# Performance work log

Hardware: AMD Instinct MI355X
Metric: run time of the kernel (lower is better)

Reference implementation:

```python
import jax, jax.numpy as jnp
import numpy as np

DIM = 512
HEADS = 8
HEAD_DIM = 64
MAX_FREQ = 256.0


def axial_freqs(H, W, head_dim, max_freq=MAX_FREQ):
    # rotary-embedding-torch: per-axis rotary dim = head_dim // 2, freqs_for='pixel'
    r = head_dim // 2
    base = jnp.linspace(1.0, max_freq / 2.0, r // 2) * jnp.pi  # (r/2,)
    ph = jnp.linspace(-1.0, 1.0, H)
    pw = jnp.linspace(-1.0, 1.0, W)
    fh = jnp.repeat(ph[:, None] * base[None, :], 2, axis=-1)  # (H, r) interleaved repeat
    fw = jnp.repeat(pw[:, None] * base[None, :], 2, axis=-1)  # (W, r)
    fh = jnp.broadcast_to(fh[:, None, :], (H, W, r))
    fw = jnp.broadcast_to(fw[None, :, :], (H, W, r))
    return jnp.concatenate([fh, fw], axis=-1)  # (H, W, head_dim)


def rotate_half(t):
    # interleaved pairs: (x1, x2) -> (-x2, x1)
    shp = t.shape
    t = t.reshape(*shp[:-1], -1, 2)
    return jnp.stack((-t[..., 1], t[..., 0]), axis=-1).reshape(shp)


def apply_rope(t, freqs):
    # freqs: (H, W, d) broadcast over (BT, h, H, W, d)
    return t * jnp.cos(freqs) + rotate_half(t) * jnp.sin(freqs)


def setup_inputs() -> dict:
    key = jax.random.key(0)
    k1, k2, k3 = jax.random.split(key, 3)
    B, T, H, W, D = 2, 8, 32, 32, DIM
    inner = HEADS * HEAD_DIM
    x = jax.random.normal(k1, (B, T, H, W, D), dtype=jnp.float32)
    w_qkv = jax.random.normal(k2, (3 * inner, D), dtype=jnp.float32) * (D ** -0.5)
    w_out = jax.random.normal(k3, (D, inner), dtype=jnp.float32) * (inner ** -0.5)
    b_out = jnp.zeros((D,), dtype=jnp.float32)
    return {"x": x, "w_qkv": w_qkv, "w_out": w_out, "b_out": b_out}


def reference(x, w_qkv, w_out, b_out):
    B, T, H, W, D = x.shape
    h, d = HEADS, HEAD_DIM
    qkv = jnp.einsum('bthwc,fc->bthwf', x, w_qkv)  # (B,T,H,W,3*inner)
    q, k, v = jnp.split(qkv, 3, axis=-1)

    def to_heads(t):
        # B T H W (h d) -> (B T) h H W d
        t = t.reshape(B * T, H, W, h, d)
        return jnp.transpose(t, (0, 3, 1, 2, 4))

    q, k, v = to_heads(q), to_heads(k), to_heads(v)
    freqs = axial_freqs(H, W, d)
    q = apply_rope(q, freqs)
    k = apply_rope(k, freqs)

    q = q.reshape(B * T, h, H * W, d)
    k = k.reshape(B * T, h, H * W, d)
    v = v.reshape(B * T, h, H * W, d)

    scale = d ** -0.5
    logits = jnp.einsum('bhnd,bhmd->bhnm', q, k) * scale
    attn = jax.nn.softmax(logits, axis=-1)
    out = jnp.einsum('bhnm,bhmd->bhnd', attn, v)  # (BT, h, HW, d)

    # (B T) h (H W) d -> B T H W (h d)
    out = out.reshape(B, T, h, H, W, d)
    out = jnp.transpose(out, (0, 1, 3, 4, 2, 5)).reshape(B, T, H, W, h * d)
    return jnp.einsum('bthwf,df->bthwd', out, w_out) + b_out
```

## Files before the change

### kernel.cpp

```cpp
#include <hip/hip_runtime.h>
#include <math.h>

#define NH 8
#define HD 64
#define NSEQ 1024
#define DMODEL 512
#define F3 1536
#define NTOK 16384
#define BH 128
#define KVP 72
#define TP 136
#define QSCALE 0.1803368867f

typedef __attribute__((ext_vector_type(8))) short bf16x8;
typedef __attribute__((ext_vector_type(4))) float f32x4;
typedef __attribute__((ext_vector_type(16))) float f32x16;
typedef __attribute__((ext_vector_type(4))) unsigned int u32x4;
#define MFMA16(a, b, c) __builtin_amdgcn_mfma_f32_16x16x32_bf16(a, b, c, 0, 0, 0)
#define MFMA32(a, b, c) __builtin_amdgcn_mfma_f32_32x32x16_bf16(a, b, c, 0, 0, 0)

__device__ __forceinline__ float freq_of(int j) {
    return 3.14159265358979323846f * (1.0f + (float)j * (127.0f / 15.0f));
}
__device__ __forceinline__ unsigned short bf16_hi(float x) {
    unsigned u = __builtin_bit_cast(unsigned, x);
    return (unsigned short)(u >> 16);
}
__device__ __forceinline__ unsigned short bf16_rtn(float x) {
    unsigned u = __builtin_bit_cast(unsigned, x);
    return (unsigned short)((u + 0x7FFF + ((u >> 16) & 1)) >> 16);
}
__device__ __forceinline__ float bf16_tofloat(unsigned short h) {
    unsigned u = ((unsigned)h) << 16;
    return __builtin_bit_cast(float, u);
}
__device__ __forceinline__ int swz(int r) { return (r & 3) ^ ((r >> 2) & 3); }

__global__ __launch_bounds__(256) void cvt_kernel(
        const float* __restrict__ src, unsigned short* __restrict__ dst) {
    const int i = blockIdx.x * 256 + threadIdx.x;
    const float4 v = ((const float4*)src)[i];
    ((ushort4*)dst)[i] = make_ushort4(bf16_rtn(v.x), bf16_rtn(v.y),
                                      bf16_rtn(v.z), bf16_rtn(v.w));
}

template<int PLANES, int NREP>
__device__ __forceinline__ void gemm_reg_pipe(
        const unsigned short* __restrict__ a_hi, const unsigned short* __restrict__ a_lo,
        const unsigned short* __restrict__ b_bf,
        char* lds, int m0, int f0, int t, f32x4 (&acc)[NREP][4][4]) {
    const int w = t >> 6, lane = t & 63, l15 = lane & 15, quad = lane >> 4;
    const int mw = (w & 1) * 64, nw = (w >> 1) * 64;
    const int APL = PLANES - 1;
    const int NPL = APL + NREP;
    const int STAGE = NPL * 4096;
    const int r = t >> 1;
    const int g0 = (t & 1) * 2;

    uint4 regs[NPL][2];
    auto load_regs = [&](int kt) {
        const int k0 = kt * 32;
        #pragma unroll
        for (int p = 0; p < NPL; p++) {
            const unsigned short* src = (p < APL) ? (p == 0 ? a_hi : a_lo) : b_bf;
            const int row0 = (p < APL) ? m0 : (f0 + (p - APL) * 128);
            const unsigned short* g = src + (size_t)(row0 + r) * DMODEL + k0 + g0 * 8;
            regs[p][0] = *(const uint4*)g;
            regs[p][1] = *(const uint4*)(g + 8);
        }
    };
    auto store_lds = [&](int stage) {
        unsigned short* S = (unsigned short*)lds + stage * STAGE;
        const int s0 = ((g0 ^ swz(r))) * 8;
        const int s1 = (((g0 + 1) ^ swz(r))) * 8;
        #pragma unroll
        for (int p = 0; p < NPL; p++) {
            unsigned short* Sp = S + p * 4096 + r * 32;
            *(uint4*)&Sp[s0] = regs[p][0];
            *(uint4*)&Sp[s1] = regs[p][1];
        }
    };

    load_regs(0);
    store_lds(0);
    for (int kt = 0; kt < 16; kt++) {
        __syncthreads();
        if (kt < 15) load_regs(kt + 1);
        const unsigned short* S = (const unsigned short*)lds + (kt & 1) * STAGE;
        bf16x8 ah[4], al[4];
        #pragma unroll
        for (int mt = 0; mt < 4; mt++) {
            const int rr = mw + mt * 16 + l15;
            const int off = rr * 32 + (quad ^ swz(rr)) * 8;
            ah[mt] = *(const bf16x8*)&S[off];
            if (APL == 2) al[mt] = *(const bf16x8*)&S[4096 + off];
        }
        #pragma unroll
        for (int nr = 0; nr < NREP; nr++) {
            bf16x8 bb[4];
            #pragma unroll
            for (int nt = 0; nt < 4; nt++) {
                const int rr = nw + nt * 16 + l15;
                bb[nt] = *(const bf16x8*)&S[(APL + nr) * 4096 + rr * 32
                                            + (quad ^ swz(rr)) * 8];
            }
            #pragma unroll
            for (int mt = 0; mt < 4; mt++)
                #pragma unroll
                for (int nt = 0; nt < 4; nt++) {
                    acc[nr][mt][nt] = MFMA16(ah[mt], bb[nt], acc[nr][mt][nt]);
                    if (APL == 2) acc[nr][mt][nt] = MFMA16(al[mt], bb[nt], acc[nr][mt][nt]);
                }
        }
        if (kt < 15) store_lds((kt + 1) & 1);
    }
    __syncthreads();
}

__device__ __forceinline__ void gemm_pipe_qkv(
        const float* __restrict__ x, const unsigned short* __restrict__ b_bf,
        char* lds, int m0, int f0, int t, f32x4 (&acc)[2][4][4]) {
    const int w = t >> 6, lane = t & 63, l15 = lane & 15, quad = lane >> 4;
    const int mw = (w & 1) * 64, nw = (w >> 1) * 64;
    const int STAGE = 4 * 4096;
    const int r = t >> 1;
    const int g0 = (t & 1) * 2;

    float4 af[4];
    uint4 bregs[2][2];
    auto load_regs = [&](int kt) {
        const int k0 = kt * 32;
        const float* gA = x + (size_t)(m0 + r) * DMODEL + k0 + g0 * 8;
        #pragma unroll
        for (int i = 0; i < 4; i++) af[i] = ((const float4*)gA)[i];
        #pragma unroll
        for (int p = 0; p < 2; p++) {
            const unsigned short* g =
                b_bf + (size_t)(f0 + p * 128 + r) * DMODEL + k0 + g0 * 8;
            bregs[p][0] = *(const uint4*)g;
            bregs[p][1] = *(const uint4*)(g + 8);
        }
    };
    auto store_lds = [&](int stage) {
        unsigned short* S = (unsigned short*)lds + stage * STAGE;
        const int s0 = ((g0 ^ swz(r))) * 8;
        const int s1 = (((g0 + 1) ^ swz(r))) * 8;
        auto cvt8 = [](const float4 a, const float4 b, uint4& hq, uint4& lq) {
            const float f[8] = {a.x, a.y, a.z, a.w, b.x, b.y, b.z, b.w};
            unsigned hw[4], lw[4];
            #pragma unroll
            for (int j = 0; j < 4; j++) {
                const unsigned u0 = __builtin_bit_cast(unsigned, f[2 * j]);
                const unsigned u1 = __builtin_bit_cast(unsigned, f[2 * j + 1]);
                const float r0 = f[2 * j]     - __builtin_bit_cast(float, u0 & 0xFFFF0000u);
                const float r1 = f[2 * j + 1] - __builtin_bit_cast(float, u1 & 0xFFFF0000u);
                hw[j] = (u0 >> 16) | (u1 & 0xFFFF0000u);
                lw[j] = (__builtin_bit_cast(unsigned, r0) >> 16)
                      | (__builtin_bit_cast(unsigned, r1) & 0xFFFF0000u);
            }
            hq = make_uint4(hw[0], hw[1], hw[2], hw[3]);
            lq = make_uint4(lw[0], lw[1], lw[2], lw[3]);
        };
        uint4 h0, l0, h1, l1;
        cvt8(af[0], af[1], h0, l0);
        cvt8(af[2], af[3], h1, l1);
        unsigned short* Sh = S + r * 32;
        unsigned short* Sl = S + 4096 + r * 32;
        *(uint4*)&Sh[s0] = h0; *(uint4*)&Sh[s1] = h1;
        *(uint4*)&Sl[s0] = l0; *(uint4*)&Sl[s1] = l1;
        #pragma unroll
        for (int p = 0; p < 2; p++) {
            unsigned short* Sp = S + (2 + p) * 4096 + r * 32;
            *(uint4*)&Sp[s0] = bregs[p][0];
            *(uint4*)&Sp[s1] = bregs[p][1];
        }
    };

    load_regs(0);
    store_lds(0);
    for (int kt = 0; kt < 16; kt++) {
        __syncthreads();
        if (kt < 15) load_regs(kt + 1);
        const unsigned short* S = (const unsigned short*)lds + (kt & 1) * STAGE;
        bf16x8 ah[4], al[4];
        #pragma unroll
        for (int mt = 0; mt < 4; mt++) {
            const int rr = mw + mt * 16 + l15;
            const int off = rr * 32 + (quad ^ swz(rr)) * 8;
            ah[mt] = *(const bf16x8*)&S[off];
            al[mt] = *(const bf16x8*)&S[4096 + off];
        }
        #pragma unroll
        for (int nr = 0; nr < 2; nr++) {
            bf16x8 bb[4];
            #pragma unroll
            for (int nt = 0; nt < 4; nt++) {
                const int rr = nw + nt * 16 + l15;
                bb[nt] = *(const bf16x8*)&S[(2 + nr) * 4096 + rr * 32
                                            + (quad ^ swz(rr)) * 8];
            }
            #pragma unroll
            for (int mt = 0; mt < 4; mt++)
                #pragma unroll
                for (int nt = 0; nt < 4; nt++) {
                    acc[nr][mt][nt] = MFMA16(ah[mt], bb[nt], acc[nr][mt][nt]);
                    acc[nr][mt][nt] = MFMA16(al[mt], bb[nt], acc[nr][mt][nt]);
                }
        }
        if (kt < 15) store_lds((kt + 1) & 1);
    }
    __syncthreads();
}

__global__ __launch_bounds__(256, 2) void qkv_mfma_kernel(
        const float* __restrict__ x, const unsigned short* __restrict__ wq_bf,
        unsigned short* __restrict__ q_bf, unsigned short* __restrict__ k_bf,
        unsigned short* __restrict__ v_th) {
    __shared__ __align__(16) char lds[65536 + 4608];
    unsigned short* T = (unsigned short*)lds;
    float* t_cy = (float*)(lds + 65536);
    float* t_sy = t_cy + 64;
    float* t_cx = t_sy + 64;
    float* t_sx = t_cx + 512;

    const int m0 = blockIdx.x * 128;
    const int f0 = blockIdx.y * 256;
    const int t = threadIdx.x;
    const int w = t >> 6, lane = t & 63, l15 = lane & 15, quad = lane >> 4;
    const int mw = (w & 1) * 64, nw = (w >> 1) * 64;
    const int sel = f0 >> 9;
    const int bt = m0 >> 10;
    const int n0 = m0 & 1023;

    if (sel != 2) {
        for (int idx = t; idx < 576; idx += 256) {
            if (idx < 64) {
                const int yi = idx >> 4, j = idx & 15;
                const float pos = -1.0f + (float)((n0 >> 5) + yi) * (2.0f / 31.0f);
                float sv, cv; sincosf(pos * freq_of(j), &sv, &cv);
                t_sy[idx] = sv; t_cy[idx] = cv;
            } else {
                const int k2 = idx - 64, xi = k2 >> 4, j = k2 & 15;
                const float pos = -1.0f + (float)xi * (2.0f / 31.0f);
                float sv, cv; sincosf(pos * freq_of(j), &sv, &cv);
                t_sx[k2] = sv; t_cx[k2] = cv;
            }
        }
    }
    __syncthreads();

    f32x4 acc[2][4][4];
    #pragma unroll
    for (int nr = 0; nr < 2; nr++)
        #pragma unroll
        for (int mt = 0; mt < 4; mt++)
            #pragma unroll
            for (int nt = 0; nt < 4; nt++) acc[nr][mt][nt] = (f32x4){0.f, 0.f, 0.f, 0.f};

    gemm_pipe_qkv(x, wq_bf, lds, m0, f0, t, acc);

    #pragma unroll
    for (int nr = 0; nr < 2; nr++) {
        const int fs = f0 + nr * 128;
        if (sel != 2) {
            const float post = (sel == 0) ? QSCALE : 1.0f;
            #pragma unroll
            for (int mt = 0; mt < 4; mt++)
                #pragma unroll
                for (int nt = 0; nt < 4; nt++)
                    #pragma unroll
                    for (int rr = 0; rr < 4; rr++) {
                        const int ml = mw + mt * 16 + quad * 4 + rr;
                        const int dd = (nw + nt * 16 + l15) & 63;
                        const int j0 = (dd & 31) >> 1;
                        float c, s;
                        if (dd < 32) { c = t_cy[(ml >> 5) * 16 + j0]; s = t_sy[(ml >> 5) * 16 + j0]; }
                        else         { c = t_cx[(ml & 31) * 16 + j0]; s = t_sx[(ml & 31) * 16 + j0]; }
                        const float v = acc[nr][mt][nt][rr];
                        const float pv = __shfl_xor(v, 1);
                        acc[nr][mt][nt][rr] =
                            ((l15 & 1) ? (v * c + pv * s) : (v * c - pv * s)) * post;
                    }
        }

        if (sel == 2) {
            #pragma unroll
            for (int mt = 0; mt < 4; mt++)
                #pragma unroll
                for (int nt = 0; nt < 4; nt++) {
                    const int fl = nw + nt * 16 + l15;
                    const int mlb = mw + mt * 16 + quad * 4;
                    ushort4 pk = make_ushort4(
                        bf16_rtn(acc[nr][mt][nt][0]), bf16_rtn(acc[nr][mt][nt][1]),
                        bf16_rtn(acc[nr][mt][nt][2]), bf16_rtn(acc[nr][mt][nt][3]));
                    *(ushort4*)&T[fl * TP + mlb] = pk;
                }
        } else {
            #pragma unroll
            for (int mt = 0; mt < 4; mt++)
                #pragma unroll
                for (int nt = 0; nt < 4; nt++)
                    #pragma unroll
                    for (int rr = 0; rr < 4; rr++) {
                        const int ml = mw + mt * 16 + quad * 4 + rr;
                        const int fl = nw + nt * 16 + l15;
                        T[ml * TP + fl] = bf16_rtn(acc[nr][mt][nt][rr]);
                    }
        }
        __syncthreads();
        if (sel == 2) {
            #pragma unroll
            for (int p = 0; p < 8; p++) {
                const int idx = p * 256 + t;
                const int fl = idx >> 4, g8 = (idx & 15) * 8;
                const int head = ((fs + fl) >> 6) & 7;
                *(uint4*)(v_th + ((size_t)(bt * NH + head) * HD + ((fs + fl) & 63)) * NSEQ
                          + n0 + g8) = *(const uint4*)&T[fl * TP + g8];
            }
        } else {
            unsigned short* dst = (sel == 0) ? q_bf : k_bf;
            #pragma unroll
            for (int p = 0; p < 8; p++) {
                const int idx = p * 256 + t;
                const int ml = idx >> 4, g8 = (idx & 15) * 8;
                const int head = ((fs + g8) >> 6) & 7;
                *(uint4*)(dst + ((size_t)(bt * NH + head) * NSEQ + n0 + ml) * HD
                          + ((fs + g8) & 63)) = *(const uint4*)&T[ml * TP + g8];
            }
        }
        __syncthreads();
    }
}

__global__ __launch_bounds__(256, 3) void attn_kernel(
        const unsigned short* __restrict__ q_bf, const unsigned short* __restrict__ k_bf,
        const unsigned short* __restrict__ v_th,
        unsigned short* __restrict__ o_bf) {
    __shared__ unsigned short Ks[2][64 * KVP];
    __shared__ unsigned short Vs[2][64 * KVP];

    const int bh = blockIdx.x;
    const int qt = blockIdx.y;
    const int t = threadIdx.x;
    const int w = t >> 6;
    const int lane = t & 63;
    const int l31 = lane & 31;
    const int hi = lane >> 5;

    const size_t bh_nd = (size_t)bh * NSEQ * HD;
    const size_t bh_dn = (size_t)bh * HD * NSEQ;

    bf16x8 qfB[4];
    {
        const size_t rbase = bh_nd + (size_t)(qt * 128 + w * 32 + l31) * HD + hi * 8;
        #pragma unroll
        for (int ds = 0; ds < 4; ds++)
            qfB[ds] = *(const bf16x8*)(q_bf + rbase + ds * 16);
    }

    uint4 kr[2], vr[2];
    auto load_kv = [&](int kt) {
        #pragma unroll
        for (int p = 0; p < 2; p++) {
            const int cc = t + p * 256;
            const int r = cc >> 3, off8 = (cc & 7) * 8;
            kr[p] = *(const uint4*)(k_bf + bh_nd + (size_t)(kt * 64 + r) * HD + off8);
            vr[p] = *(const uint4*)(v_th + bh_dn + (size_t)r * NSEQ + kt * 64 + off8);
        }
    };
    auto store_kv = [&](int st) {
        #pragma unroll
        for (int p = 0; p < 2; p++) {
            const int cc = t + p * 256;
            const int r = cc >> 3, off8 = (cc & 7) * 8;
            *(uint4*)&Ks[st][r * KVP + off8] = kr[p];
            *(uint4*)&Vs[st][r * KVP + off8] = vr[p];
        }
    };

    const bf16x8 ones = {(short)0x3F80, (short)0x3F80, (short)0x3F80, (short)0x3F80,
                         (short)0x3F80, (short)0x3F80, (short)0x3F80, (short)0x3F80};

    f32x16 o_acc[2], l_acc;
    #pragma unroll
    for (int i = 0; i < 16; i++) {
        o_acc[0][i] = 0.f; o_acc[1][i] = 0.f; l_acc[i] = 0.f;
    }

    load_kv(0);
    store_kv(0);
    for (int kt = 0; kt < 16; kt++) {
        __syncthreads();
        if (kt < 15) load_kv(kt + 1);
        const unsigned short* K = Ks[kt & 1];
        const unsigned short* V = Vs[kt & 1];

        #pragma unroll
        for (int nt2 = 0; nt2 < 2; nt2++) {
            f32x16 s;
            #pragma unroll
            for (int i = 0; i < 16; i++) s[i] = 0.f;
            #pragma unroll
            for (int ds = 0; ds < 4; ds++) {
                const bf16x8 kb =
                    *(const bf16x8*)&K[(nt2 * 32 + l31) * KVP + ds * 16 + hi * 8];
                s = MFMA32(kb, qfB[ds], s);
            }

            unsigned wv[8];
            #pragma unroll
            for (int i = 0; i < 8; i++) {
                const float p0 = exp2f(s[2 * i]);
                const float p1 = exp2f(s[2 * i + 1]);
                asm("v_cvt_pk_bf16_f32 %0, %1, %2" : "=v"(wv[i]) : "v"(p0), "v"(p1));
            }
            asm volatile("v_permlane32_swap_b32 %0, %1" : "+v"(wv[0]), "+v"(wv[2]));
            asm volatile("v_permlane32_swap_b32 %0, %1" : "+v"(wv[1]), "+v"(wv[3]));
            asm volatile("v_permlane32_swap_b32 %0, %1" : "+v"(wv[4]), "+v"(wv[6]));
            asm volatile("v_permlane32_swap_b32 %0, %1" : "+v"(wv[5]), "+v"(wv[7]));

            #pragma unroll
            for (int k2 = 0; k2 < 2; k2++) {
                const u32x4 paw = {wv[k2 * 4 + 0], wv[k2 * 4 + 1],
                                   wv[k2 * 4 + 2], wv[k2 * 4 + 3]};
                const bf16x8 pa = __builtin_bit_cast(bf16x8, paw);
                const int kstep = nt2 * 2 + k2;
                l_acc = MFMA32(pa, ones, l_acc);
                #pragma unroll
                for (int dt = 0; dt < 2; dt++) {
                    const bf16x8 vb =
                        *(const bf16x8*)&V[(dt * 32 + l31) * KVP + kstep * 16 + hi * 8];
                    o_acc[dt] = MFMA32(pa, vb, o_acc[dt]);
                }
            }
        }
        if (kt < 15) store_kv((kt + 1) & 1);
    }

    __syncthreads();
    unsigned short* Osh = &Ks[0][0];
    #pragma unroll
    for (int r = 0; r < 16; r++) {
        const float inv = 1.0f / l_acc[r];
        const int row = w * 32 + (r & 3) + 8 * (r >> 2) + 4 * hi;
        #pragma unroll
        for (int dt = 0; dt < 2; dt++)
            Osh[row * KVP + dt * 32 + l31] = bf16_rtn(o_acc[dt][r] * inv);
    }
    __syncthreads();
    const int btq = bh >> 3, head = bh & 7;
    #pragma unroll
    for (int p = 0; p < 4; p++) {
        const int idx = p * 256 + t;
        const int row = idx >> 3, g8 = (idx & 7) * 8;
        *(uint4*)(o_bf + ((size_t)(btq * NSEQ + qt * 128 + row)) * DMODEL
                  + head * HD + g8) = *(const uint4*)&Osh[row * KVP + g8];
    }
}

__global__ __launch_bounds__(256, 3) void proj_mfma_kernel(
        const unsigned short* __restrict__ o_bf,
        const unsigned short* __restrict__ wo_bf,
        const float* __restrict__ b_out, float* __restrict__ out) {
    __shared__ __align__(16) char lds[32768];

    const int m0 = blockIdx.x * 128;
    const int f0 = blockIdx.y * 128;
    const int t = threadIdx.x;
    const int w = t >> 6, lane = t & 63, l15 = lane & 15, quad = lane >> 4;
    const int mw = (w & 1) * 64, nw = (w >> 1) * 64;

    f32x4 acc[1][4][4];
    #pragma unroll
    for (int mt = 0; mt < 4; mt++)
        #pragma unroll
        for (int nt = 0; nt < 4; nt++) acc[0][mt][nt] = (f32x4){0.f, 0.f, 0.f, 0.f};

    gemm_reg_pipe<2, 1>(o_bf, o_bf, wo_bf, lds, m0, f0, t, acc);

    float bias_v[4];
    #pragma unroll
    for (int nt = 0; nt < 4; nt++) bias_v[nt] = b_out[f0 + nw + nt * 16 + l15];
    #pragma unroll
    for (int mt = 0; mt < 4; mt++)
        #pragma unroll
        for (int nt = 0; nt < 4; nt++)
            #pragma unroll
            for (int rr = 0; rr < 4; rr++) {
                const int m = m0 + mw + mt * 16 + quad * 4 + rr;
                out[(size_t)m * DMODEL + f0 + nw + nt * 16 + l15] =
                    acc[0][mt][nt][rr] + bias_v[nt];
            }
}

extern "C" void kernel_launch(void* const* d_in, const int* in_sizes, int n_in,
                              void* d_out, int out_size, void* d_ws, size_t ws_size,
                              hipStream_t stream) {
    const float* x  = (const float*)d_in[0];
    const float* wq = (const float*)d_in[1];
    const float* wo = (const float*)d_in[2];
    const float* bo = (const float*)d_in[3];
    float* out = (float*)d_out;

    const size_t per = (size_t)BH * NSEQ * HD;
    unsigned short* o_bf = (unsigned short*)d_ws;
    unsigned short* q_bf = o_bf + per;
    unsigned short* k_bf = q_bf + per;
    unsigned short* v_th = k_bf + per;
    unsigned short* wq_bf = v_th + per;
    unsigned short* wo_bf = wq_bf + (size_t)F3 * DMODEL;

    cvt_kernel<<<dim3(F3 * DMODEL / 1024), 256, 0, stream>>>(wq, wq_bf);
    cvt_kernel<<<dim3(DMODEL * DMODEL / 1024), 256, 0, stream>>>(wo, wo_bf);
    qkv_mfma_kernel<<<dim3(NTOK / 128, F3 / 256), 256, 0, stream>>>(
        x, wq_bf, q_bf, k_bf, v_th);
    attn_kernel<<<dim3(BH, 8), 256, 0, stream>>>(
        q_bf, k_bf, v_th, o_bf);
    proj_mfma_kernel<<<dim3(NTOK / 128, DMODEL / 128), 256, 0, stream>>>(
        o_bf, wo_bf, bo, out);
}
```

Before: 250.5 us.

## Double per-block query tile in attention, widen proj N tile, merge weight converts

Each attention wave now processes two 32-row query fragments, so every K and V fragment loaded from LDS feeds twice as many MFMAs, and the grid halves to 4 query tiles of 256 rows. The output projection now computes a 128x256 tile per block using the register pipeline with two N replicas, and its LDS grows to 48KB. The two weight-conversion launches are merged into a single kernel. The cost is more registers (launch bounds lowered to 2 blocks per SM), lower occupancy, and fewer blocks for the GPU to schedule.

Measured after the change: 234.3 us. -6.5%, faster.

```diff
diff --git a/kernel.cpp b/kernel.cpp
--- a/kernel.cpp
+++ b/kernel.cpp
@@ -22,23 +22,21 @@
 __device__ __forceinline__ float freq_of(int j) {
     return 3.14159265358979323846f * (1.0f + (float)j * (127.0f / 15.0f));
 }
-__device__ __forceinline__ unsigned short bf16_hi(float x) {
-    unsigned u = __builtin_bit_cast(unsigned, x);
-    return (unsigned short)(u >> 16);
-}
 __device__ __forceinline__ unsigned short bf16_rtn(float x) {
     unsigned u = __builtin_bit_cast(unsigned, x);
     return (unsigned short)((u + 0x7FFF + ((u >> 16) & 1)) >> 16);
 }
-__device__ __forceinline__ float bf16_tofloat(unsigned short h) {
-    unsigned u = ((unsigned)h) << 16;
-    return __builtin_bit_cast(float, u);
-}
 __device__ __forceinline__ int swz(int r) { return (r & 3) ^ ((r >> 2) & 3); }
 
-__global__ __launch_bounds__(256) void cvt_kernel(
-        const float* __restrict__ src, unsigned short* __restrict__ dst) {
-    const int i = blockIdx.x * 256 + threadIdx.x;
+__global__ __launch_bounds__(256) void cvt2_kernel(
+        const float* __restrict__ wq, unsigned short* __restrict__ wq_bf,
+        const float* __restrict__ wo, unsigned short* __restrict__ wo_bf) {
+    const int b = blockIdx.x;
+    const float* src;
+    unsigned short* dst;
+    int i;
+    if (b < F3 * DMODEL / 1024) { src = wq; dst = wq_bf; i = b * 256 + threadIdx.x; }
+    else { src = wo; dst = wo_bf; i = (b - F3 * DMODEL / 1024) * 256 + threadIdx.x; }
     const float4 v = ((const float4*)src)[i];
     ((ushort4*)dst)[i] = make_ushort4(bf16_rtn(v.x), bf16_rtn(v.y),
                                       bf16_rtn(v.z), bf16_rtn(v.w));
@@ -332,7 +330,7 @@
     }
 }
 
-__global__ __launch_bounds__(256, 3) void attn_kernel(
+__global__ __launch_bounds__(256, 2) void attn_kernel(
         const unsigned short* __restrict__ q_bf, const unsigned short* __restrict__ k_bf,
         const unsigned short* __restrict__ v_th,
         unsigned short* __restrict__ o_bf) {
@@ -350,12 +348,14 @@
     const size_t bh_nd = (size_t)bh * NSEQ * HD;
     const size_t bh_dn = (size_t)bh * HD * NSEQ;
 
-    bf16x8 qfB[4];
-    {
-        const size_t rbase = bh_nd + (size_t)(qt * 128 + w * 32 + l31) * HD + hi * 8;
+    bf16x8 qfB[2][4];
+    #pragma unroll
+    for (int mf = 0; mf < 2; mf++) {
+        const size_t rbase =
+            bh_nd + (size_t)(qt * 256 + w * 64 + mf * 32 + l31) * HD + hi * 8;
         #pragma unroll
         for (int ds = 0; ds < 4; ds++)
-            qfB[ds] = *(const bf16x8*)(q_bf + rbase + ds * 16);
+            qfB[mf][ds] = *(const bf16x8*)(q_bf + rbase + ds * 16);
     }
 
     uint4 kr[2], vr[2];
@@ -381,10 +381,12 @@
     const bf16x8 ones = {(short)0x3F80, (short)0x3F80, (short)0x3F80, (short)0x3F80,
                          (short)0x3F80, (short)0x3F80, (short)0x3F80, (short)0x3F80};
 
-    f32x16 o_acc[2], l_acc;
+    f32x16 o_acc[2][2], l_acc[2];
     #pragma unroll
     for (int i = 0; i < 16; i++) {
-        o_acc[0][i] = 0.f; o_acc[1][i] = 0.f; l_acc[i] = 0.f;
+        o_acc[0][0][i] = 0.f; o_acc[0][1][i] = 0.f;
+        o_acc[1][0][i] = 0.f; o_acc[1][1][i] = 0.f;
+        l_acc[0][i] = 0.f; l_acc[1][i] = 0.f;
     }
 
     load_kv(0);
@@ -397,40 +399,49 @@
 
         #pragma unroll
         for (int nt2 = 0; nt2 < 2; nt2++) {
-            f32x16 s;
-            #pragma unroll
-            for (int i = 0; i < 16; i++) s[i] = 0.f;
-            #pragma unroll
-            for (int ds = 0; ds < 4; ds++) {
-                const bf16x8 kb =
-                    *(const bf16x8*)&K[(nt2 * 32 + l31) * KVP + ds * 16 + hi * 8];
-                s = MFMA32(kb, qfB[ds], s);
-            }
-
-            unsigned wv[8];
-            #pragma unroll
-            for (int i = 0; i < 8; i++) {
-                const float p0 = exp2f(s[2 * i]);
-                const float p1 = exp2f(s[2 * i + 1]);
-                asm("v_cvt_pk_bf16_f32 %0, %1, %2" : "=v"(wv[i]) : "v"(p0), "v"(p1));
-            }
-            asm volatile("v_permlane32_swap_b32 %0, %1" : "+v"(wv[0]), "+v"(wv[2]));
-            asm volatile("v_permlane32_swap_b32 %0, %1" : "+v"(wv[1]), "+v"(wv[3]));
-            asm volatile("v_permlane32_swap_b32 %0, %1" : "+v"(wv[4]), "+v"(wv[6]));
-            asm volatile("v_permlane32_swap_b32 %0, %1" : "+v"(wv[5]), "+v"(wv[7]));
+            bf16x8 kb[4];
+            #pragma unroll
+            for (int ds = 0; ds < 4; ds++)
+                kb[ds] = *(const bf16x8*)&K[(nt2 * 32 + l31) * KVP + ds * 16 + hi * 8];
+
+            u32x4 paw[2][2];
+            #pragma unroll
+            for (int mf = 0; mf < 2; mf++) {
+                f32x16 s;
+                #pragma unroll
+                for (int i = 0; i < 16; i++) s[i] = 0.f;
+                #pragma unroll
+                for (int ds = 0; ds < 4; ds++) s = MFMA32(kb[ds], qfB[mf][ds], s);
+
+                unsigned wv[8];
+                #pragma unroll
+                for (int i = 0; i < 8; i++) {
+                    const float p0 = exp2f(s[2 * i]);
+                    const float p1 = exp2f(s[2 * i + 1]);
+                    asm("v_cvt_pk_bf16_f32 %0, %1, %2" : "=v"(wv[i]) : "v"(p0), "v"(p1));
+                }
+                asm volatile("v_permlane32_swap_b32 %0, %1" : "+v"(wv[0]), "+v"(wv[2]));
+                asm volatile("v_permlane32_swap_b32 %0, %1" : "+v"(wv[1]), "+v"(wv[3]));
+                asm volatile("v_permlane32_swap_b32 %0, %1" : "+v"(wv[4]), "+v"(wv[6]));
+                asm volatile("v_permlane32_swap_b32 %0, %1" : "+v"(wv[5]), "+v"(wv[7]));
+                paw[mf][0] = (u32x4){wv[0], wv[1], wv[2], wv[3]};
+                paw[mf][1] = (u32x4){wv[4], wv[5], wv[6], wv[7]};
+            }
 
             #pragma unroll
             for (int k2 = 0; k2 < 2; k2++) {
-                const u32x4 paw = {wv[k2 * 4 + 0], wv[k2 * 4 + 1],
-                                   wv[k2 * 4 + 2], wv[k2 * 4 + 3]};
-                const bf16x8 pa = __builtin_bit_cast(bf16x8, paw);
-                const int kstep = nt2 * 2 + k2;
-                l_acc = MFMA32(pa, ones, l_acc);
-                #pragma unroll
-                for (int dt = 0; dt < 2; dt++) {
-                    const bf16x8 vb =
-                        *(const bf16x8*)&V[(dt * 32 + l31) * KVP + kstep * 16 + hi * 8];
-                    o_acc[dt] = MFMA32(pa, vb, o_acc[dt]);
+                bf16x8 vb[2];
+                #pragma unroll
+                for (int dt = 0; dt < 2; dt++)
+                    vb[dt] = *(const bf16x8*)&V[(dt * 32 + l31) * KVP
+                                 + (nt2 * 2 + k2) * 16 + hi * 8];
+                #pragma unroll
+                for (int mf = 0; mf < 2; mf++) {
+                    const bf16x8 pa = __builtin_bit_cast(bf16x8, paw[mf][k2]);
+                    l_acc[mf] = MFMA32(pa, ones, l_acc[mf]);
+                    #pragma unroll
+                    for (int dt = 0; dt < 2; dt++)
+                        o_acc[mf][dt] = MFMA32(pa, vb[dt], o_acc[mf][dt]);
                 }
             }
         }
@@ -440,57 +451,65 @@
     __syncthreads();
     unsigned short* Osh = &Ks[0][0];
     #pragma unroll
-    for (int r = 0; r < 16; r++) {
-        const float inv = 1.0f / l_acc[r];
-        const int row = w * 32 + (r & 3) + 8 * (r >> 2) + 4 * hi;
-        #pragma unroll
-        for (int dt = 0; dt < 2; dt++)
-            Osh[row * KVP + dt * 32 + l31] = bf16_rtn(o_acc[dt][r] * inv);
-    }
+    for (int mf = 0; mf < 2; mf++)
+        #pragma unroll
+        for (int r = 0; r < 16; r++) {
+            const float inv = 1.0f / l_acc[mf][r];
+            const int row = w * 64 + mf * 32 + (r & 3) + 8 * (r >> 2) + 4 * hi;
+            #pragma unroll
+            for (int dt = 0; dt < 2; dt++)
+                Osh[row * KVP + dt * 32 + l31] = bf16_rtn(o_acc[mf][dt][r] * inv);
+        }
     __syncthreads();
     const int btq = bh >> 3, head = bh & 7;
     #pragma unroll
-    for (int p = 0; p < 4; p++) {
+    for (int p = 0; p < 8; p++) {
         const int idx = p * 256 + t;
         const int row = idx >> 3, g8 = (idx & 7) * 8;
-        *(uint4*)(o_bf + ((size_t)(btq * NSEQ + qt * 128 + row)) * DMODEL
+        *(uint4*)(o_bf + ((size_t)(btq * NSEQ + qt * 256 + row)) * DMODEL
                   + head * HD + g8) = *(const uint4*)&Osh[row * KVP + g8];
     }
 }
 
-__global__ __launch_bounds__(256, 3) void proj_mfma_kernel(
+__global__ __launch_bounds__(256, 2) void proj_mfma_kernel(
         const unsigned short* __restrict__ o_bf,
         const unsigned short* __restrict__ wo_bf,
         const float* __restrict__ b_out, float* __restrict__ out) {
-    __shared__ __align__(16) char lds[32768];
+    __shared__ __align__(16) char lds[49152];
 
     const int m0 = blockIdx.x * 128;
-    const int f0 = blockIdx.y * 128;
+    const int f0 = blockIdx.y * 256;
     const int t = threadIdx.x;
     const int w = t >> 6, lane = t & 63, l15 = lane & 15, quad = lane >> 4;
     const int mw = (w & 1) * 64, nw = (w >> 1) * 64;
 
-    f32x4 acc[1][4][4];
-    #pragma unroll
-    for (int mt = 0; mt < 4; mt++)
-        #pragma unroll
-        for (int nt = 0; nt < 4; nt++) acc[0][mt][nt] = (f32x4){0.f, 0.f, 0.f, 0.f};
-
-    gemm_reg_pipe<2, 1>(o_bf, o_bf, wo_bf, lds, m0, f0, t, acc);
-
-    float bias_v[4];
-    #pragma unroll
-    for (int nt = 0; nt < 4; nt++) bias_v[nt] = b_out[f0 + nw + nt * 16 + l15];
-    #pragma unroll
-    for (int mt = 0; mt < 4; mt++)
-        #pragma unroll
-        for (int nt = 0; nt < 4; nt++)
-            #pragma unroll
-            for (int rr = 0; rr < 4; rr++) {
-                const int m = m0 + mw + mt * 16 + quad * 4 + rr;
-                out[(size_t)m * DMODEL + f0 + nw + nt * 16 + l15] =
-                    acc[0][mt][nt][rr] + bias_v[nt];
-            }
+    f32x4 acc[2][4][4];
+    #pragma unroll
+    for (int nr = 0; nr < 2; nr++)
+        #pragma unroll
+        for (int mt = 0; mt < 4; mt++)
+            #pragma unroll
+            for (int nt = 0; nt < 4; nt++) acc[nr][mt][nt] = (f32x4){0.f, 0.f, 0.f, 0.f};
+
+    gemm_reg_pipe<2, 2>(o_bf, o_bf, wo_bf, lds, m0, f0, t, acc);
+
+    #pragma unroll
+    for (int nr = 0; nr < 2; nr++) {
+        const int fs = f0 + nr * 128;
+        float bias_v[4];
+        #pragma unroll
+        for (int nt = 0; nt < 4; nt++) bias_v[nt] = b_out[fs + nw + nt * 16 + l15];
+        #pragma unroll
+        for (int mt = 0; mt < 4; mt++)
+            #pragma unroll
+            for (int nt = 0; nt < 4; nt++)
+                #pragma unroll
+                for (int rr = 0; rr < 4; rr++) {
+                    const int m = m0 + mw + mt * 16 + quad * 4 + rr;
+                    out[(size_t)m * DMODEL + fs + nw + nt * 16 + l15] =
+                        acc[nr][mt][nt][rr] + bias_v[nt];
+                }
+    }
 }
 
 extern "C" void kernel_launch(void* const* d_in, const int* in_sizes, int n_in,
@@ -510,12 +529,12 @@
     unsigned short* wq_bf = v_th + per;
     unsigned short* wo_bf = wq_bf + (size_t)F3 * DMODEL;
 
-    cvt_kernel<<<dim3(F3 * DMODEL / 1024), 256, 0, stream>>>(wq, wq_bf);
-    cvt_kernel<<<dim3(DMODEL * DMODEL / 1024), 256, 0, stream>>>(wo, wo_bf);
+    cvt2_kernel<<<dim3((F3 * DMODEL + DMODEL * DMODEL) / 1024), 256, 0, stream>>>(
+        wq, wq_bf, wo, wo_bf);
     qkv_mfma_kernel<<<dim3(NTOK / 128, F3 / 256), 256, 0, stream>>>(
         x, wq_bf, q_bf, k_bf, v_th);
-    attn_kernel<<<dim3(BH, 8), 256, 0, stream>>>(
+    attn_kernel<<<dim3(BH, 4), 256, 0, stream>>>(
         q_bf, k_bf, v_th, o_bf);
-    proj_mfma_kernel<<<dim3(NTOK / 128, DMODEL / 128), 256, 0, stream>>>(
+    proj_mfma_kernel<<<dim3(NTOK / 128, DMODEL / 256), 256, 0, stream>>>(
         o_bf, wo_bf, bo, out);
 }
```
